# Performance work log

Measured on AMD Instinct MI355X. Metric: run time of the kernel, lower is better.

## Reference

```python
import jax, jax.numpy as jnp
import numpy as np

SELF_OBS_DIM = 18
NEIGHBOR_OBS_DIM = 6
HIDDEN = 256
NUM_NEIGHBORS = 6
BATCH = 131072


def setup_inputs() -> dict:
    key = jax.random.key(0)
    k1, k2, k3, k4, k5, k6 = jax.random.split(key, 6)
    obs_dim = SELF_OBS_DIM + NEIGHBOR_OBS_DIM * NUM_NEIGHBORS
    self_obs = jax.random.normal(k1, (BATCH, SELF_OBS_DIM), dtype=jnp.float32)
    obs = jax.random.normal(k2, (BATCH, obs_dim), dtype=jnp.float32)
    # MLP params (PyTorch Linear default init scale ~ 1/sqrt(fan_in))
    W1 = jax.random.uniform(k3, (NEIGHBOR_OBS_DIM, HIDDEN), minval=-1.0, maxval=1.0) / np.sqrt(NEIGHBOR_OBS_DIM)
    b1 = jax.random.uniform(k4, (HIDDEN,), minval=-1.0, maxval=1.0) / np.sqrt(NEIGHBOR_OBS_DIM)
    W2 = jax.random.uniform(k5, (HIDDEN, HIDDEN), minval=-1.0, maxval=1.0) / np.sqrt(HIDDEN)
    b2 = jax.random.uniform(k6, (HIDDEN,), minval=-1.0, maxval=1.0) / np.sqrt(HIDDEN)
    return {
        "self_obs": self_obs,
        "obs": obs,
        "W1": W1.astype(jnp.float32),
        "b1": b1.astype(jnp.float32),
        "W2": W2.astype(jnp.float32),
        "b2": b2.astype(jnp.float32),
        "all_neighbor_obs_size": NEIGHBOR_OBS_DIM * NUM_NEIGHBORS,
        "batch_size": BATCH,
    }


def reference(self_obs, obs, W1, b1, W2, b2, all_neighbor_obs_size, batch_size):
    # slice out neighbor observations: obs[:, self_obs_dim : self_obs_dim + all_neighbor_obs_size]
    obs_neighbors = obs[:, SELF_OBS_DIM:SELF_OBS_DIM + all_neighbor_obs_size]
    # reshape to per-neighbor rows: [B * num_neighbors, neighbor_obs_dim]
    x = obs_neighbors.reshape(-1, NEIGHBOR_OBS_DIM)
    # shared 2-layer MLP with tanh (sample-factory default nonlinearity)
    h = jnp.tanh(x @ W1 + b1)
    h = jnp.tanh(h @ W2 + b2)
    # [B, num_neighbors, hidden] -> mean over neighbor axis
    neighbor_embeds = h.reshape(batch_size, -1, HIDDEN)
    mean_embed = jnp.mean(neighbor_embeds, axis=1)
    return mean_embed
```

## Files before the change

kernel.cpp:

```cpp
#include <hip/hip_runtime.h>


#define HID     256
#define OBSD    54
#define SELFD   18
#define TILE_B  8
#define TILE_R  48
#define LDA     264
#define LDH     260
#define BATCHN  131072
#define NTILES  (BATCHN / TILE_B)
#define GRID_WG 2048

typedef __attribute__((ext_vector_type(8))) short bf16x8;
typedef __attribute__((ext_vector_type(4))) short s16x4;
typedef __attribute__((ext_vector_type(4))) float f32x4;

__device__ __forceinline__ float fast_tanh(float x) {
    float t = __builtin_amdgcn_exp2f(x * 2.8853900817779268f);
    return 1.0f - 2.0f * __builtin_amdgcn_rcpf(t + 1.0f);
}

__device__ __forceinline__ short f2bf(float f) {
    unsigned u = __float_as_uint(f);
    u += 0x7fffu + ((u >> 16) & 1u);
    return (short)(u >> 16);
}

__global__ void prep_w2t(const float* __restrict__ w2, short* __restrict__ w2t) {
    int idx = blockIdx.x * 256 + threadIdx.x;
    int n = idx >> 8;
    int k = idx & 255;
    w2t[idx] = f2bf(w2[k * 256 + n]);
}

__global__ __launch_bounds__(256, 2) void qenc_main(
        const float* __restrict__ obs,
        const float* __restrict__ W1,
        const float* __restrict__ b1,
        const short* __restrict__ w2t,
        const float* __restrict__ b2,
        float* __restrict__ out)
{
    __shared__ union {
        short a[TILE_R * LDA];
        float h[TILE_R * LDH];
    } u;
    __shared__ float xt[TILE_B * 36];

    const int tid  = threadIdx.x;
    const int wave = tid >> 6;
    const int lane = tid & 63;
    const int q    = lane >> 4;
    const int c16  = lane & 15;

    bf16x8 Bf[8][4];
    #pragma unroll
    for (int kk = 0; kk < 8; ++kk) {
        #pragma unroll
        for (int ct = 0; ct < 4; ++ct) {
            const int n = wave * 64 + ct * 16 + c16;
            const int k = kk * 32 + q * 8;
            Bf[kk][ct] = *(const bf16x8*)(w2t + n * 256 + k);
        }
    }

    const int j0 = (tid & 63) * 4;
    const int rg = wave;
    float w1r[6][4], b1r[4], b2r[4];
    #pragma unroll
    for (int k = 0; k < 6; ++k)
        #pragma unroll
        for (int c = 0; c < 4; ++c) w1r[k][c] = W1[k * 256 + j0 + c];
    #pragma unroll
    for (int c = 0; c < 4; ++c) b1r[c] = b1[j0 + c];
    #pragma unroll
    for (int ct = 0; ct < 4; ++ct) b2r[ct] = b2[wave * 64 + ct * 16 + c16];

    for (int tile = blockIdx.x; tile < NTILES; tile += gridDim.x) {
        const int b0 = tile * TILE_B;

        for (int i = tid; i < TILE_B * 36; i += 256) {
            const int b = i / 36, o = i - b * 36;
            xt[i] = obs[(b0 + b) * OBSD + SELFD + o];
        }
        __syncthreads();

        #pragma unroll
        for (int i = 0; i < 12; ++i) {
            const int r  = rg + i * 4;
            const int bl = r / 6;
            const int nn = r - bl * 6;
            const float* xv = &xt[bl * 36 + nn * 6];
            short hs[4];
            #pragma unroll
            for (int c = 0; c < 4; ++c) {
                float s = b1r[c];
                #pragma unroll
                for (int k = 0; k < 6; ++k) s = fmaf(xv[k], w1r[k][c], s);
                hs[c] = f2bf(fast_tanh(s));
            }
            *(s16x4*)&u.a[r * LDA + j0] = (s16x4){hs[0], hs[1], hs[2], hs[3]};
        }
        __syncthreads();

        f32x4 acc[3][4];
        #pragma unroll
        for (int rt = 0; rt < 3; ++rt)
            #pragma unroll
            for (int ct = 0; ct < 4; ++ct) acc[rt][ct] = (f32x4){0.f, 0.f, 0.f, 0.f};

        #pragma unroll
        for (int kk = 0; kk < 8; ++kk) {
            bf16x8 Af[3];
            #pragma unroll
            for (int rt = 0; rt < 3; ++rt)
                Af[rt] = *(const bf16x8*)&u.a[(rt * 16 + c16) * LDA + kk * 32 + q * 8];
            #pragma unroll
            for (int rt = 0; rt < 3; ++rt)
                #pragma unroll
                for (int ct = 0; ct < 4; ++ct)
                    acc[rt][ct] = __builtin_amdgcn_mfma_f32_16x16x32_bf16(
                        Af[rt], Bf[kk][ct], acc[rt][ct], 0, 0, 0);
        }
        __syncthreads();

        #pragma unroll
        for (int rt = 0; rt < 3; ++rt) {
            #pragma unroll
            for (int ct = 0; ct < 4; ++ct) {
                const int col = wave * 64 + ct * 16 + c16;
                #pragma unroll
                for (int g = 0; g < 4; ++g) {
                    const int row = rt * 16 + q * 4 + g;
                    u.h[row * LDH + col] = fast_tanh(acc[rt][ct][g] + b2r[ct]);
                }
            }
        }
        __syncthreads();

        #pragma unroll
        for (int bl = 0; bl < TILE_B; ++bl) {
            float s = 0.f;
            #pragma unroll
            for (int n = 0; n < 6; ++n) s += u.h[(bl * 6 + n) * LDH + tid];
            out[(b0 + bl) * HID + tid] = s * (1.0f / 6.0f);
        }
    }
}

extern "C" void kernel_launch(void* const* d_in, const int* in_sizes, int n_in,
                              void* d_out, int out_size, void* d_ws, size_t ws_size,
                              hipStream_t stream) {
    const float* obs = (const float*)d_in[1];
    const float* W1  = (const float*)d_in[2];
    const float* b1  = (const float*)d_in[3];
    const float* W2  = (const float*)d_in[4];
    const float* b2  = (const float*)d_in[5];
    float* outp = (float*)d_out;
    short* w2t  = (short*)d_ws;

    prep_w2t<<<256, 256, 0, stream>>>(W2, w2t);
    qenc_main<<<GRID_WG, 256, 0, stream>>>(obs, W1, b1, w2t, b2, outp);
}
```

Before: 394.1 us.

## Move layer-1 to MFMA, stream W2 fragments from cache, raise occupancy

Layer 1 now runs on bf16 MFMA using a zero-padded transposed W1 built in the prep kernel, instead of scalar FMAs. W2 fragments are read from global/L2 for each k-step rather than held in 128 registers, which lets launch bounds go to 4 workgroups per CU. The layer-2 output is written to LDS as transposed packed bf16, so the neighbor mean reads three 32-bit words per output. The intent is higher occupancy and fewer VALU instructions. The cost is repeated W2 loads from cache every tile and bf16 rounding of the inputs and hidden activations, which lowers accuracy.

Measured after the change: 537.7 us. 36.5% more time.

```diff
diff --git a/kernel.cpp b/kernel.cpp
--- a/kernel.cpp
+++ b/kernel.cpp
@@ -6,14 +6,14 @@
 #define SELFD   18
 #define TILE_B  8
 #define TILE_R  48
+#define LDX     40
 #define LDA     264
-#define LDH     260
+#define LDH     54
 #define BATCHN  131072
 #define NTILES  (BATCHN / TILE_B)
 #define GRID_WG 2048
 
 typedef __attribute__((ext_vector_type(8))) short bf16x8;
-typedef __attribute__((ext_vector_type(4))) short s16x4;
 typedef __attribute__((ext_vector_type(4))) float f32x4;
 
 __device__ __forceinline__ float fast_tanh(float x) {
@@ -21,86 +21,98 @@
     return 1.0f - 2.0f * __builtin_amdgcn_rcpf(t + 1.0f);
 }
 
-__device__ __forceinline__ short f2bf(float f) {
+__device__ __forceinline__ unsigned bfbits(float f) {
     unsigned u = __float_as_uint(f);
     u += 0x7fffu + ((u >> 16) & 1u);
-    return (short)(u >> 16);
+    return u >> 16;
 }
 
-__global__ void prep_w2t(const float* __restrict__ w2, short* __restrict__ w2t) {
+__global__ void prep(const float* __restrict__ W1, const float* __restrict__ W2,
+                     short* __restrict__ w1t, short* __restrict__ w2t) {
     int idx = blockIdx.x * 256 + threadIdx.x;
-    int n = idx >> 8;
-    int k = idx & 255;
-    w2t[idx] = f2bf(w2[k * 256 + n]);
+    if (idx < 65536) {
+        int n = idx >> 8, k = idx & 255;
+        w2t[idx] = (short)bfbits(W2[k * HID + n]);
+    } else {
+        int j = idx - 65536;
+        int n = j >> 5, k = j & 31;
+        w1t[j] = (k < 6) ? (short)bfbits(W1[k * HID + n]) : (short)0;
+    }
 }
 
-__global__ __launch_bounds__(256, 2) void qenc_main(
+__global__ __launch_bounds__(256, 4) void qenc_main(
         const float* __restrict__ obs,
-        const float* __restrict__ W1,
+        const short* __restrict__ w1t,
         const float* __restrict__ b1,
         const short* __restrict__ w2t,
         const float* __restrict__ b2,
         float* __restrict__ out)
 {
+    __shared__ short xt[TILE_R * LDX];
     __shared__ union {
         short a[TILE_R * LDA];
-        float h[TILE_R * LDH];
+        short ht[HID * LDH];
     } u;
-    __shared__ float xt[TILE_B * 36];
 
     const int tid  = threadIdx.x;
     const int wave = tid >> 6;
     const int lane = tid & 63;
     const int q    = lane >> 4;
     const int c16  = lane & 15;
+    const int colbase = wave * 64;
 
-    bf16x8 Bf[8][4];
+    float b1r[4], b2r[4];
     #pragma unroll
-    for (int kk = 0; kk < 8; ++kk) {
-        #pragma unroll
-        for (int ct = 0; ct < 4; ++ct) {
-            const int n = wave * 64 + ct * 16 + c16;
-            const int k = kk * 32 + q * 8;
-            Bf[kk][ct] = *(const bf16x8*)(w2t + n * 256 + k);
-        }
+    for (int ct = 0; ct < 4; ++ct) {
+        b1r[ct] = b1[colbase + ct * 16 + c16];
+        b2r[ct] = b2[colbase + ct * 16 + c16];
     }
 
-    const int j0 = (tid & 63) * 4;
-    const int rg = wave;
-    float w1r[6][4], b1r[4], b2r[4];
-    #pragma unroll
-    for (int k = 0; k < 6; ++k)
-        #pragma unroll
-        for (int c = 0; c < 4; ++c) w1r[k][c] = W1[k * 256 + j0 + c];
-    #pragma unroll
-    for (int c = 0; c < 4; ++c) b1r[c] = b1[j0 + c];
-    #pragma unroll
-    for (int ct = 0; ct < 4; ++ct) b2r[ct] = b2[wave * 64 + ct * 16 + c16];
+    const short* w2l = w2t + (colbase + c16) * HID + q * 8;
+    const short* w1l = w1t + (colbase + c16) * 32 + q * 8;
 
-    for (int tile = blockIdx.x; tile < NTILES; tile += gridDim.x) {
+    for (int tile = blockIdx.x; tile < NTILES; tile += GRID_WG) {
         const int b0 = tile * TILE_B;
 
-        for (int i = tid; i < TILE_B * 36; i += 256) {
-            const int b = i / 36, o = i - b * 36;
-            xt[i] = obs[(b0 + b) * OBSD + SELFD + o];
+        if (tid < 96) {
+            int r = tid >> 1, h = tid & 1;
+            if (h == 0) {
+                int bl = r / 6, nn = r - bl * 6;
+                const float* src = obs + (size_t)(b0 + bl) * OBSD + SELFD + nn * 6;
+                bf16x8 v;
+                #pragma unroll
+                for (int k = 0; k < 6; ++k) v[k] = (short)bfbits(src[k]);
+                v[6] = 0; v[7] = 0;
+                *(bf16x8*)&xt[r * LDX] = v;
+            } else {
+                bf16x8 z = {0, 0, 0, 0, 0, 0, 0, 0};
+                *(bf16x8*)&xt[r * LDX + 8]  = z;
+                *(bf16x8*)&xt[r * LDX + 16] = z;
+                *(bf16x8*)&xt[r * LDX + 24] = z;
+            }
         }
         __syncthreads();
 
-        #pragma unroll
-        for (int i = 0; i < 12; ++i) {
-            const int r  = rg + i * 4;
-            const int bl = r / 6;
-            const int nn = r - bl * 6;
-            const float* xv = &xt[bl * 36 + nn * 6];
-            short hs[4];
+        {
+            bf16x8 Ax[3];
             #pragma unroll
-            for (int c = 0; c < 4; ++c) {
-                float s = b1r[c];
+            for (int rt = 0; rt < 3; ++rt)
+                Ax[rt] = *(const bf16x8*)&xt[(rt * 16 + c16) * LDX + q * 8];
+            #pragma unroll
+            for (int ct = 0; ct < 4; ++ct) {
+                bf16x8 B1f = *(const bf16x8*)(w1l + ct * 16 * 32);
                 #pragma unroll
-                for (int k = 0; k < 6; ++k) s = fmaf(xv[k], w1r[k][c], s);
-                hs[c] = f2bf(fast_tanh(s));
+                for (int rt = 0; rt < 3; ++rt) {
+                    f32x4 c = __builtin_amdgcn_mfma_f32_16x16x32_bf16(
+                        Ax[rt], B1f, (f32x4){0.f, 0.f, 0.f, 0.f}, 0, 0, 0);
+                    #pragma unroll
+                    for (int g = 0; g < 4; ++g) {
+                        float hv = fast_tanh(c[g] + b1r[ct]);
+                        u.a[(rt * 16 + q * 4 + g) * LDA + colbase + ct * 16 + c16]
+                            = (short)bfbits(hv);
+                    }
+                }
             }
-            *(s16x4*)&u.a[r * LDA + j0] = (s16x4){hs[0], hs[1], hs[2], hs[3]};
         }
         __syncthreads();
 
@@ -112,7 +124,10 @@
 
         #pragma unroll
         for (int kk = 0; kk < 8; ++kk) {
-            bf16x8 Af[3];
+            bf16x8 Bf[4], Af[3];
+            #pragma unroll
+            for (int ct = 0; ct < 4; ++ct)
+                Bf[ct] = *(const bf16x8*)(w2l + ct * 16 * HID + kk * 32);
             #pragma unroll
             for (int rt = 0; rt < 3; ++rt)
                 Af[rt] = *(const bf16x8*)&u.a[(rt * 16 + c16) * LDA + kk * 32 + q * 8];
@@ -121,30 +136,38 @@
                 #pragma unroll
                 for (int ct = 0; ct < 4; ++ct)
                     acc[rt][ct] = __builtin_amdgcn_mfma_f32_16x16x32_bf16(
-                        Af[rt], Bf[kk][ct], acc[rt][ct], 0, 0, 0);
+                        Af[rt], Bf[ct], acc[rt][ct], 0, 0, 0);
         }
         __syncthreads();
 
         #pragma unroll
-        for (int rt = 0; rt < 3; ++rt) {
+        for (int ct = 0; ct < 4; ++ct) {
+            const int col = colbase + ct * 16 + c16;
             #pragma unroll
-            for (int ct = 0; ct < 4; ++ct) {
-                const int col = wave * 64 + ct * 16 + c16;
-                #pragma unroll
-                for (int g = 0; g < 4; ++g) {
-                    const int row = rt * 16 + q * 4 + g;
-                    u.h[row * LDH + col] = fast_tanh(acc[rt][ct][g] + b2r[ct]);
-                }
+            for (int rt = 0; rt < 3; ++rt) {
+                float t0 = fast_tanh(acc[rt][ct][0] + b2r[ct]);
+                float t1 = fast_tanh(acc[rt][ct][1] + b2r[ct]);
+                float t2 = fast_tanh(acc[rt][ct][2] + b2r[ct]);
+                float t3 = fast_tanh(acc[rt][ct][3] + b2r[ct]);
+                const int row = rt * 16 + q * 4;
+                unsigned d0 = bfbits(t0) | (bfbits(t1) << 16);
+                unsigned d1 = bfbits(t2) | (bfbits(t3) << 16);
+                *(unsigned*)&u.ht[col * LDH + row]     = d0;
+                *(unsigned*)&u.ht[col * LDH + row + 2] = d1;
             }
         }
         __syncthreads();
 
         #pragma unroll
         for (int bl = 0; bl < TILE_B; ++bl) {
+            const unsigned* p = (const unsigned*)&u.ht[tid * LDH + bl * 6];
             float s = 0.f;
             #pragma unroll
-            for (int n = 0; n < 6; ++n) s += u.h[(bl * 6 + n) * LDH + tid];
-            out[(b0 + bl) * HID + tid] = s * (1.0f / 6.0f);
+            for (int d = 0; d < 3; ++d) {
+                unsigned uu = p[d];
+                s += __uint_as_float(uu << 16) + __uint_as_float(uu & 0xffff0000u);
+            }
+            out[(size_t)(b0 + bl) * HID + tid] = s * (1.0f / 6.0f);
         }
     }
 }
@@ -158,8 +181,10 @@
     const float* W2  = (const float*)d_in[4];
     const float* b2  = (const float*)d_in[5];
     float* outp = (float*)d_out;
-    short* w2t  = (short*)d_ws;
 
-    prep_w2t<<<256, 256, 0, stream>>>(W2, w2t);
-    qenc_main<<<GRID_WG, 256, 0, stream>>>(obs, W1, b1, w2t, b2, outp);
+    short* w2t = (short*)d_ws;
+    short* w1t = (short*)((char*)d_ws + 131072);
+
+    prep<<<288, 256, 0, stream>>>(W1, W2, w1t, w2t);
+    qenc_main<<<GRID_WG, 256, 0, stream>>>(obs, w1t, b1, w2t, b2, outp);
 }
```
